# Performance work log

Measured on AMD Instinct MI355X. Metric: run time of the kernel, lower is better.

The kernel has to match this reference:

```python
import jax, jax.numpy as jnp
import numpy as np

# Dims: original code requires bond_dim == feature_dim (it contracts the bond
# axis of the running vector against the per-site feature vector).
B, N, F = 2048, 128, 64   # batch, num_sites, feature_dim
D = 64                    # bond_dim (== F by structural requirement)


def setup_inputs() -> dict:
    key = jax.random.key(0)
    k1, k2, k3, k4 = jax.random.split(key, 4)
    # scale weights so the chain of 126 bilinear contractions stays O(1)
    s = 1.0 / np.sqrt(D * F).astype(np.float32)
    x = jax.random.normal(k1, (B, N, F), dtype=jnp.float32)
    w0 = jax.random.normal(k2, (F, D), dtype=jnp.float32) / np.sqrt(F).astype(np.float32)
    w_mid = jax.random.normal(k3, (N - 2, D, F, D), dtype=jnp.float32) * s
    w_last = jax.random.normal(k4, (D, F), dtype=jnp.float32) * s
    return {"x": x, "w0": w0, "w_mid": w_mid, "w_last": w_last}


def reference(x, w0, w_mid, w_last):
    # Site 0: v[b,d] = sum_f x[b,0,f] * w0[f,d]
    v = jnp.einsum('bf,fd->bd', x[:, 0], w0)
    # Middle sites, batched across samples (replaces tf.map_fn + python loop).
    # Faithful to original: tensordot(v, W_i, [[-1],[0]]) -> [f,e], then
    # tensordot(., x_i, [[-1],[0]]) contracts the BOND axis e with x_i.
    xs = jnp.swapaxes(x[:, 1:-1], 0, 1)  # [N-2, B, F]

    def step(v, args):
        Wi, xi = args  # Wi: [D,F,D], xi: [B,F]
        v = jnp.einsum('bd,dfe,be->bf', v, Wi, xi)
        return v, None

    v, _ = jax.lax.scan(step, v, (w_mid, xs))
    # Last site: tensordot(v, w_last, [[-1],[0]]) -> [F]; then dot with x[-1]
    out = jnp.einsum('bd,df,bf->b', v, w_last, x[:, -1])  # [B]
    return out
```

## Files before the change

### kernel.cpp

```cpp
#include <hip/hip_runtime.h>
#include <stdint.h>
#include <stddef.h>


typedef _Float16 half8   __attribute__((ext_vector_type(8)));
typedef _Float16 half2_t __attribute__((ext_vector_type(2)));
typedef float    floatx4 __attribute__((ext_vector_type(4)));

#define WP_BYTES  66060288u
#define P_ELEMS   524288
#define BSTRIDE   131072

__device__ inline half2_t h2of(half8 v, int j) {
  half2_t r; r[0] = v[2*j]; r[1] = v[2*j+1]; return r;
}
__device__ inline half8 cvt8(floatx4 a, floatx4 b) {
  half8 o;
  o[0]=(_Float16)a[0]; o[1]=(_Float16)a[1]; o[2]=(_Float16)a[2]; o[3]=(_Float16)a[3];
  o[4]=(_Float16)b[0]; o[5]=(_Float16)b[1]; o[6]=(_Float16)b[2]; o[7]=(_Float16)b[3];
  return o;
}

__global__ void prep_wp(const float* __restrict__ wm, _Float16* __restrict__ Wp) {
  const int t  = blockIdx.x * 256 + threadIdx.x;
  const int kg = t & 3;
  const int f  = (t >> 2) & 63;
  const int kt = (t >> 8) & 127;
  const int s  = t >> 15;
  const int d  = kt >> 1;
  const int e0 = (kt & 1) * 32 + kg * 8;
  const float* src = wm + ((((size_t)s * 64 + d) * 64 + f) * 64 + e0);
  floatx4 a = *(const floatx4*)src;
  floatx4 b = *(const floatx4*)(src + 4);
  *(half8*)(Wp + (size_t)t * 8) = cvt8(a, b);
}

__global__ void prep_v0(const float* __restrict__ x, const float* __restrict__ w0,
                        float* __restrict__ v0) {
  const int b = blockIdx.x * 4 + (threadIdx.x >> 6);
  const int d = threadIdx.x & 63;
  const float* xr = x + (size_t)b * 8192;
  float s = 0.f;
  #pragma unroll
  for (int f = 0; f < 64; ++f) s += xr[f] * w0[f * 64 + d];
  v0[b * 64 + d] = s;
}

__global__ __launch_bounds__(256) void site_step(
    const _Float16* __restrict__ Wp, const float* __restrict__ x,
    const float* __restrict__ uprev, float* __restrict__ upart,
    int s, int nprev)
{
  __shared__ float ub[64 * 17];
  __shared__ float red[4 * 64 * 68];

  const int tid = threadIdx.x;
  const int w = tid >> 6, lane = tid & 63;
  const int c15 = lane & 15, kg = lane >> 4;
  const int kq = (int)blockIdx.x & 3, bt = (int)blockIdx.x >> 2;
  const int b0 = bt * 64;
  const int xsite = s + 1;

  for (int t = tid; t < 1024; t += 256) {
    const int bb = t >> 4, dl = t & 15;
    const int gi = (b0 + bb) * 64 + kq * 16 + dl;
    float v;
    if (nprev == 1) v = uprev[gi];
    else v = uprev[gi] + uprev[BSTRIDE + gi] + uprev[2*BSTRIDE + gi] + uprev[3*BSTRIDE + gi];
    ub[bb * 17 + dl] = v;
  }
  __syncthreads();

  half8 xA[4], xB[4];
  #pragma unroll
  for (int mt = 0; mt < 4; ++mt) {
    const float* xp = x + ((size_t)(b0 + mt * 16 + c15) * 128 + xsite) * 64 + kg * 8;
    xA[mt] = cvt8(*(const floatx4*)xp,        *(const floatx4*)(xp + 4));
    xB[mt] = cvt8(*(const floatx4*)(xp + 32), *(const floatx4*)(xp + 36));
  }

  floatx4 C[4][4] = {};
  const int ktbase = kq * 32 + w * 8;
  const _Float16* wbase = Wp + ((size_t)s * 128 + ktbase) * 2048;
  #pragma unroll
  for (int kt = 0; kt < 8; ++kt) {
    const int dl = w * 4 + (kt >> 1);
    half8 bf[4];
    #pragma unroll
    for (int nt = 0; nt < 4; ++nt)
      bf[nt] = *(const half8*)(wbase + ((size_t)kt * 64 + nt * 16 + c15) * 32 + kg * 8);
    #pragma unroll
    for (int mt = 0; mt < 4; ++mt) {
      const float us = ub[(mt * 16 + c15) * 17 + dl];
      const _Float16 uh = (_Float16)us;
      half2_t uu; uu[0] = uh; uu[1] = uh;
      const half8 xc = (kt & 1) ? xB[mt] : xA[mt];
      half2_t p0 = uu * h2of(xc, 0), p1 = uu * h2of(xc, 1);
      half2_t p2 = uu * h2of(xc, 2), p3 = uu * h2of(xc, 3);
      half8 af;
      af[0]=p0[0]; af[1]=p0[1]; af[2]=p1[0]; af[3]=p1[1];
      af[4]=p2[0]; af[5]=p2[1]; af[6]=p3[0]; af[7]=p3[1];
      #pragma unroll
      for (int nt = 0; nt < 4; ++nt)
        C[mt][nt] = __builtin_amdgcn_mfma_f32_16x16x32_f16(af, bf[nt], C[mt][nt], 0, 0, 0);
    }
  }

  #pragma unroll
  for (int mt = 0; mt < 4; ++mt)
    #pragma unroll
    for (int nt = 0; nt < 4; ++nt)
      #pragma unroll
      for (int r = 0; r < 4; ++r)
        red[(w * 64 + mt * 16 + kg * 4 + r) * 68 + nt * 16 + c15] = C[mt][nt][r];
  __syncthreads();

  {
    const int bb = tid >> 2, f0 = (tid & 3) * 16;
    float* op = upart + (size_t)kq * BSTRIDE + (size_t)(b0 + bb) * 64 + f0;
    #pragma unroll
    for (int q = 0; q < 4; ++q) {
      floatx4 a0 = *(const floatx4*)&red[(0 * 64 + bb) * 68 + f0 + q * 4];
      floatx4 a1 = *(const floatx4*)&red[(1 * 64 + bb) * 68 + f0 + q * 4];
      floatx4 a2 = *(const floatx4*)&red[(2 * 64 + bb) * 68 + f0 + q * 4];
      floatx4 a3 = *(const floatx4*)&red[(3 * 64 + bb) * 68 + f0 + q * 4];
      *(floatx4*)(op + q * 4) = a0 + a1 + a2 + a3;
    }
  }
}

__global__ void finalize(const float* __restrict__ part, const float* __restrict__ x,
                         const float* __restrict__ wlast, float* __restrict__ out) {
  const int w = threadIdx.x >> 6, lane = threadIdx.x & 63;
  const int b = (int)blockIdx.x * 4 + w;
  const size_t gi = (size_t)b * 64 + lane;
  const float u = part[gi] + part[BSTRIDE + gi] + part[2*BSTRIDE + gi] + part[3*BSTRIDE + gi];
  const float* xr = x + (size_t)b * 8192 + 127 * 64;
  const float* wr = wlast + lane * 64;
  float z = 0.f;
  #pragma unroll
  for (int f = 0; f < 64; f += 4) {
    floatx4 wv = *(const floatx4*)(wr + f);
    floatx4 xv = *(const floatx4*)(xr + f);
    z += wv[0]*xv[0] + wv[1]*xv[1] + wv[2]*xv[2] + wv[3]*xv[3];
  }
  float p = u * z;
  #pragma unroll
  for (int m = 32; m; m >>= 1) p += __shfl_xor(p, m, 64);
  if (lane == 0) out[b] = p;
}

extern "C" void kernel_launch(void* const* d_in, const int* in_sizes, int n_in,
                              void* d_out, int out_size, void* d_ws, size_t ws_size,
                              hipStream_t stream) {
  const float* x     = (const float*)d_in[0];
  const float* w0    = (const float*)d_in[1];
  const float* wmid  = (const float*)d_in[2];
  const float* wlast = (const float*)d_in[3];
  float* out = (float*)d_out;

  _Float16* Wp  = (_Float16*)d_ws;
  float* part0  = (float*)((char*)d_ws + WP_BYTES);
  float* part1  = part0 + P_ELEMS;
  float* v0     = part1 + P_ELEMS;

  prep_wp<<<16128, 256, 0, stream>>>(wmid, Wp);
  prep_v0<<<512,   256, 0, stream>>>(x, w0, v0);

  for (int s = 0; s < 126; ++s) {
    const float* up = (s == 0) ? v0 : ((s & 1) ? part0 : part1);
    float* po = (s & 1) ? part1 : part0;
    site_step<<<128, 256, 0, stream>>>(Wp, x, up, po, s, (s == 0) ? 1 : 4);
  }
  finalize<<<512, 256, 0, stream>>>(part1, x, wlast, out);
}
```

Baseline: 1.560 ms.

## Fuse all site steps into one persistent kernel with grid barriers

Replaces the 126 per-site kernel launches and the finalize launch with a single persistent kernel of 128 workgroups that loops over sites. Workgroups synchronise between sites through a global atomic counter barrier, and partial sums are exchanged with agent-scope atomic loads and stores. The change also prefetches the first weight fragment of the next site before the barrier, and halves the LDS reduction buffer by reducing in two phases. The goal is to remove per-launch overhead and tail gaps, at the cost of spin-wait barrier latency and a requirement that all 128 workgroups are co-resident.

```diff
diff --git a/kernel.cpp b/kernel.cpp
--- a/kernel.cpp
+++ b/kernel.cpp
@@ -10,6 +10,7 @@
 #define WP_BYTES  66060288u
 #define P_ELEMS   524288
 #define BSTRIDE   131072
+#define NWG       128
 
 __device__ inline half2_t h2of(half8 v, int j) {
   half2_t r; r[0] = v[2*j]; r[1] = v[2*j+1]; return r;
@@ -19,6 +20,12 @@
   o[0]=(_Float16)a[0]; o[1]=(_Float16)a[1]; o[2]=(_Float16)a[2]; o[3]=(_Float16)a[3];
   o[4]=(_Float16)b[0]; o[5]=(_Float16)b[1]; o[6]=(_Float16)b[2]; o[7]=(_Float16)b[3];
   return o;
+}
+__device__ inline float ld_agent(const float* p) {
+  return __hip_atomic_load((float*)p, __ATOMIC_RELAXED, __HIP_MEMORY_SCOPE_AGENT);
+}
+__device__ inline void st_agent(float* p, float v) {
+  __hip_atomic_store(p, v, __ATOMIC_RELAXED, __HIP_MEMORY_SCOPE_AGENT);
 }
 
 __global__ void prep_wp(const float* __restrict__ wm, _Float16* __restrict__ Wp) {
@@ -46,108 +53,165 @@
   v0[b * 64 + d] = s;
 }
 
-__global__ __launch_bounds__(256) void site_step(
+__device__ inline void gridbar(unsigned* cnt, unsigned* gen, unsigned target) {
+  __syncthreads();
+  if (threadIdx.x == 0) {
+    __threadfence();
+    unsigned prev = __hip_atomic_fetch_add(cnt, 1u, __ATOMIC_ACQ_REL,
+                                           __HIP_MEMORY_SCOPE_AGENT);
+    if (prev == NWG - 1u) {
+      __hip_atomic_store(cnt, 0u, __ATOMIC_RELAXED, __HIP_MEMORY_SCOPE_AGENT);
+      __hip_atomic_store(gen, target, __ATOMIC_RELEASE, __HIP_MEMORY_SCOPE_AGENT);
+    } else {
+      while (__hip_atomic_load(gen, __ATOMIC_ACQUIRE, __HIP_MEMORY_SCOPE_AGENT)
+             < target)
+        __builtin_amdgcn_s_sleep(8);
+    }
+  }
+  __syncthreads();
+}
+
+__global__ __launch_bounds__(256, 1) void mps_chain(
     const _Float16* __restrict__ Wp, const float* __restrict__ x,
-    const float* __restrict__ uprev, float* __restrict__ upart,
-    int s, int nprev)
+    const float* __restrict__ v0, const float* __restrict__ wlast,
+    float* __restrict__ part0, float* __restrict__ part1,
+    unsigned* __restrict__ bar, float* __restrict__ out)
 {
   __shared__ float ub[64 * 17];
-  __shared__ float red[4 * 64 * 68];
+  __shared__ float red[4 * 32 * 68];
 
   const int tid = threadIdx.x;
   const int w = tid >> 6, lane = tid & 63;
   const int c15 = lane & 15, kg = lane >> 4;
   const int kq = (int)blockIdx.x & 3, bt = (int)blockIdx.x >> 2;
   const int b0 = bt * 64;
-  const int xsite = s + 1;
-
-  for (int t = tid; t < 1024; t += 256) {
-    const int bb = t >> 4, dl = t & 15;
-    const int gi = (b0 + bb) * 64 + kq * 16 + dl;
-    float v;
-    if (nprev == 1) v = uprev[gi];
-    else v = uprev[gi] + uprev[BSTRIDE + gi] + uprev[2*BSTRIDE + gi] + uprev[3*BSTRIDE + gi];
-    ub[bb * 17 + dl] = v;
-  }
-  __syncthreads();
-
-  half8 xA[4], xB[4];
-  #pragma unroll
-  for (int mt = 0; mt < 4; ++mt) {
-    const float* xp = x + ((size_t)(b0 + mt * 16 + c15) * 128 + xsite) * 64 + kg * 8;
-    xA[mt] = cvt8(*(const floatx4*)xp,        *(const floatx4*)(xp + 4));
-    xB[mt] = cvt8(*(const floatx4*)(xp + 32), *(const floatx4*)(xp + 36));
+  unsigned* cnt = bar;
+  unsigned* gen = bar + 16;
+
+  const int ktbase = kq * 32 + w * 8;
+
+  half8 pf[4];
+  {
+    const _Float16* wb0 = Wp + (size_t)ktbase * 2048;
+    #pragma unroll
+    for (int nt = 0; nt < 4; ++nt)
+      pf[nt] = *(const half8*)(wb0 + ((size_t)nt * 16 + c15) * 32 + kg * 8);
   }
 
   floatx4 C[4][4] = {};
-  const int ktbase = kq * 32 + w * 8;
-  const _Float16* wbase = Wp + ((size_t)s * 128 + ktbase) * 2048;
-  #pragma unroll
-  for (int kt = 0; kt < 8; ++kt) {
-    const int dl = w * 4 + (kt >> 1);
-    half8 bf[4];
-    #pragma unroll
-    for (int nt = 0; nt < 4; ++nt)
-      bf[nt] = *(const half8*)(wbase + ((size_t)kt * 64 + nt * 16 + c15) * 32 + kg * 8);
+  #pragma unroll 1
+  for (int s = 0; s < 126; ++s) {
+    const float* up = (s == 0) ? v0 : ((s & 1) ? part0 : part1);
+    float* po = (s & 1) ? part1 : part0;
+
+    #pragma unroll
+    for (int k = 0; k < 4; ++k) {
+      const int li = tid + k * 256;
+      const int bb = li >> 4, dl = li & 15;
+      const int gi = (b0 + bb) * 64 + kq * 16 + dl;
+      float v;
+      if (s == 0) v = ld_agent(up + gi);
+      else v = ld_agent(up + gi) + ld_agent(up + BSTRIDE + gi)
+             + ld_agent(up + 2 * BSTRIDE + gi) + ld_agent(up + 3 * BSTRIDE + gi);
+      ub[bb * 17 + dl] = v;
+    }
+    __syncthreads();
+
+    const int xsite = s + 1;
+    half8 xA[4], xB[4];
     #pragma unroll
     for (int mt = 0; mt < 4; ++mt) {
-      const float us = ub[(mt * 16 + c15) * 17 + dl];
-      const _Float16 uh = (_Float16)us;
-      half2_t uu; uu[0] = uh; uu[1] = uh;
-      const half8 xc = (kt & 1) ? xB[mt] : xA[mt];
-      half2_t p0 = uu * h2of(xc, 0), p1 = uu * h2of(xc, 1);
-      half2_t p2 = uu * h2of(xc, 2), p3 = uu * h2of(xc, 3);
-      half8 af;
-      af[0]=p0[0]; af[1]=p0[1]; af[2]=p1[0]; af[3]=p1[1];
-      af[4]=p2[0]; af[5]=p2[1]; af[6]=p3[0]; af[7]=p3[1];
+      const float* xp = x + ((size_t)(b0 + mt * 16 + c15) * 128 + xsite) * 64 + kg * 8;
+      xA[mt] = cvt8(*(const floatx4*)xp,        *(const floatx4*)(xp + 4));
+      xB[mt] = cvt8(*(const floatx4*)(xp + 32), *(const floatx4*)(xp + 36));
+    }
+
+    const _Float16* wbase = Wp + ((size_t)s * 128 + ktbase) * 2048;
+    #pragma unroll
+    for (int kt = 0; kt < 8; ++kt) {
+      const int dl = w * 4 + (kt >> 1);
+      half8 bf[4];
+      if (kt == 0) {
+        #pragma unroll
+        for (int nt = 0; nt < 4; ++nt) bf[nt] = pf[nt];
+      } else {
+        #pragma unroll
+        for (int nt = 0; nt < 4; ++nt)
+          bf[nt] = *(const half8*)(wbase + ((size_t)kt * 64 + nt * 16 + c15) * 32 + kg * 8);
+      }
+      #pragma unroll
+      for (int mt = 0; mt < 4; ++mt) {
+        const float us = ub[(mt * 16 + c15) * 17 + dl];
+        const _Float16 uh = (_Float16)us;
+        half2_t uu; uu[0] = uh; uu[1] = uh;
+        const half8 xc = (kt & 1) ? xB[mt] : xA[mt];
+        half2_t p0 = uu * h2of(xc, 0), p1 = uu * h2of(xc, 1);
+        half2_t p2 = uu * h2of(xc, 2), p3 = uu * h2of(xc, 3);
+        half8 af;
+        af[0]=p0[0]; af[1]=p0[1]; af[2]=p1[0]; af[3]=p1[1];
+        af[4]=p2[0]; af[5]=p2[1]; af[6]=p3[0]; af[7]=p3[1];
+        #pragma unroll
+        for (int nt = 0; nt < 4; ++nt)
+          C[mt][nt] = __builtin_amdgcn_mfma_f32_16x16x32_f16(af, bf[nt], C[mt][nt], 0, 0, 0);
+      }
+    }
+
+    if (s + 1 < 126) {
+      const _Float16* wbn = Wp + ((size_t)(s + 1) * 128 + ktbase) * 2048;
       #pragma unroll
       for (int nt = 0; nt < 4; ++nt)
-        C[mt][nt] = __builtin_amdgcn_mfma_f32_16x16x32_f16(af, bf[nt], C[mt][nt], 0, 0, 0);
-    }
-  }
-
-  #pragma unroll
-  for (int mt = 0; mt < 4; ++mt)
-    #pragma unroll
-    for (int nt = 0; nt < 4; ++nt)
-      #pragma unroll
-      for (int r = 0; r < 4; ++r)
-        red[(w * 64 + mt * 16 + kg * 4 + r) * 68 + nt * 16 + c15] = C[mt][nt][r];
-  __syncthreads();
-
-  {
-    const int bb = tid >> 2, f0 = (tid & 3) * 16;
-    float* op = upart + (size_t)kq * BSTRIDE + (size_t)(b0 + bb) * 64 + f0;
-    #pragma unroll
-    for (int q = 0; q < 4; ++q) {
-      floatx4 a0 = *(const floatx4*)&red[(0 * 64 + bb) * 68 + f0 + q * 4];
-      floatx4 a1 = *(const floatx4*)&red[(1 * 64 + bb) * 68 + f0 + q * 4];
-      floatx4 a2 = *(const floatx4*)&red[(2 * 64 + bb) * 68 + f0 + q * 4];
-      floatx4 a3 = *(const floatx4*)&red[(3 * 64 + bb) * 68 + f0 + q * 4];
-      *(floatx4*)(op + q * 4) = a0 + a1 + a2 + a3;
-    }
-  }
-}
-
-__global__ void finalize(const float* __restrict__ part, const float* __restrict__ x,
-                         const float* __restrict__ wlast, float* __restrict__ out) {
-  const int w = threadIdx.x >> 6, lane = threadIdx.x & 63;
-  const int b = (int)blockIdx.x * 4 + w;
-  const size_t gi = (size_t)b * 64 + lane;
-  const float u = part[gi] + part[BSTRIDE + gi] + part[2*BSTRIDE + gi] + part[3*BSTRIDE + gi];
-  const float* xr = x + (size_t)b * 8192 + 127 * 64;
-  const float* wr = wlast + lane * 64;
-  float z = 0.f;
-  #pragma unroll
-  for (int f = 0; f < 64; f += 4) {
-    floatx4 wv = *(const floatx4*)(wr + f);
-    floatx4 xv = *(const floatx4*)(xr + f);
-    z += wv[0]*xv[0] + wv[1]*xv[1] + wv[2]*xv[2] + wv[3]*xv[3];
-  }
-  float p = u * z;
-  #pragma unroll
-  for (int m = 32; m; m >>= 1) p += __shfl_xor(p, m, 64);
-  if (lane == 0) out[b] = p;
+        pf[nt] = *(const half8*)(wbn + ((size_t)nt * 16 + c15) * 32 + kg * 8);
+    }
+
+    #pragma unroll
+    for (int ph = 0; ph < 2; ++ph) {
+      #pragma unroll
+      for (int m2 = 0; m2 < 2; ++m2) {
+        const int mt = ph * 2 + m2;
+        #pragma unroll
+        for (int nt = 0; nt < 4; ++nt) {
+          #pragma unroll
+          for (int r = 0; r < 4; ++r)
+            red[(w * 32 + m2 * 16 + kg * 4 + r) * 68 + nt * 16 + c15] = C[mt][nt][r];
+          C[mt][nt] = (floatx4){0.f, 0.f, 0.f, 0.f};
+        }
+      }
+      __syncthreads();
+      #pragma unroll
+      for (int k = 0; k < 8; ++k) {
+        const int li = tid + k * 256;
+        const int bb = li >> 6, f = li & 63;
+        const float sum = red[(0 * 32 + bb) * 68 + f] + red[(1 * 32 + bb) * 68 + f]
+                        + red[(2 * 32 + bb) * 68 + f] + red[(3 * 32 + bb) * 68 + f];
+        st_agent(po + (size_t)kq * BSTRIDE + (size_t)(b0 + ph * 32 + bb) * 64 + f, sum);
+      }
+      __syncthreads();
+    }
+
+    gridbar(cnt, gen, (unsigned)(s + 1));
+  }
+
+  if (kq == 0) {
+    for (int bb = w; bb < 64; bb += 4) {
+      const int b = b0 + bb;
+      const size_t gi = (size_t)b * 64 + lane;
+      const float u = ld_agent(part1 + gi) + ld_agent(part1 + BSTRIDE + gi)
+                    + ld_agent(part1 + 2 * BSTRIDE + gi) + ld_agent(part1 + 3 * BSTRIDE + gi);
+      const float* xr = x + (size_t)b * 8192 + 127 * 64;
+      const float* wr = wlast + lane * 64;
+      float z = 0.f;
+      #pragma unroll
+      for (int f = 0; f < 64; f += 4) {
+        floatx4 wv = *(const floatx4*)(wr + f);
+        floatx4 xv = *(const floatx4*)(xr + f);
+        z += wv[0]*xv[0] + wv[1]*xv[1] + wv[2]*xv[2] + wv[3]*xv[3];
+      }
+      float p = u * z;
+      #pragma unroll
+      for (int m = 32; m; m >>= 1) p += __shfl_xor(p, m, 64);
+      if (lane == 0) out[b] = p;
+    }
+  }
 }
 
 extern "C" void kernel_launch(void* const* d_in, const int* in_sizes, int n_in,
@@ -163,14 +227,11 @@
   float* part0  = (float*)((char*)d_ws + WP_BYTES);
   float* part1  = part0 + P_ELEMS;
   float* v0     = part1 + P_ELEMS;
+  unsigned* bar = (unsigned*)(v0 + 131072);
 
   prep_wp<<<16128, 256, 0, stream>>>(wmid, Wp);
   prep_v0<<<512,   256, 0, stream>>>(x, w0, v0);
-
-  for (int s = 0; s < 126; ++s) {
-    const float* up = (s == 0) ? v0 : ((s & 1) ? part0 : part1);
-    float* po = (s & 1) ? part1 : part0;
-    site_step<<<128, 256, 0, stream>>>(Wp, x, up, po, s, (s == 0) ? 1 : 4);
-  }
-  finalize<<<512, 256, 0, stream>>>(part1, x, wlast, out);
-}
+  hipMemsetAsync(bar, 0, 256, stream);
+
+  mps_chain<<<NWG, 256, 0, stream>>>(Wp, x, v0, wlast, part0, part1, bar, out);
+}
```

New measurement: 2.282 ms. +46.3%, slower.
